# Optimization experiments

Hardware: AMD Instinct MI355X
Metric: run time of the kernel (lower is better)

The kernel has to match this reference:

```python
import jax, jax.numpy as jnp
import numpy as np

NUM_HEADS = 32
NUM_KV_HEADS = 2
HEAD_DIM = 128
ROTARY_DIM = 64  # partial_rotary_factor 0.5 * head_dim
HIDDEN = 4096
SEQ = 2048


def _rotate_half_interleaved(x):
    # rotates pairs (x0,x1)->(-x1,x0) interleaved, matching torch rotate_half above
    x1 = x[..., 0::2]
    x2 = x[..., 1::2]
    return jnp.stack((-x2, x1), axis=-1).reshape(x.shape)


def _apply_rope(q, k, cos, sin):
    # q: [S, Hq, D], k: [S, Hkv, D], cos/sin: [S, ROTARY_DIM]
    # torch code: take first half of cos/sin then repeat_interleave(2) -> length ROTARY_DIM
    cos_i = jnp.repeat(cos[:, : ROTARY_DIM // 2], 2, axis=-1)[:, None, :]  # [S,1,RD]
    sin_i = jnp.repeat(sin[:, : ROTARY_DIM // 2], 2, axis=-1)[:, None, :]
    q_rot, q_pass = q[..., :ROTARY_DIM], q[..., ROTARY_DIM:]
    k_rot, k_pass = k[..., :ROTARY_DIM], k[..., ROTARY_DIM:]
    q_rot = q_rot * cos_i + _rotate_half_interleaved(q_rot) * sin_i
    k_rot = k_rot * cos_i + _rotate_half_interleaved(k_rot) * sin_i
    return jnp.concatenate([q_rot, q_pass], -1), jnp.concatenate([k_rot, k_pass], -1)


def setup_inputs() -> dict:
    key = jax.random.key(0)
    ks = jax.random.split(key, 6)
    S = SEQ
    qkv_out = (NUM_HEADS + 2 * NUM_KV_HEADS) * HEAD_DIM  # 4608
    hidden_states = jax.random.normal(ks[0], (S, HIDDEN), jnp.float32)
    # realistic rope angles
    inv_freq = 1.0 / (10000.0 ** (np.arange(0, ROTARY_DIM, 2, dtype=np.float32) / ROTARY_DIM))
    ang = np.arange(S, dtype=np.float32)[:, None] * inv_freq[None, :]  # [S, RD/2]
    ang = np.concatenate([ang, ang], axis=-1)  # [S, RD]
    cos = jnp.asarray(np.cos(ang))
    sin = jnp.asarray(np.sin(ang))
    w_qkv = jax.random.normal(ks[1], (HIDDEN, qkv_out), jnp.float32) * 0.02
    b_qkv = jax.random.normal(ks[2], (qkv_out,), jnp.float32) * 0.02
    w_o = jax.random.normal(ks[3], (NUM_HEADS * HEAD_DIM, HIDDEN), jnp.float32) * 0.02
    return {"hidden_states": hidden_states, "cos": cos, "sin": sin,
            "w_qkv": w_qkv, "b_qkv": b_qkv, "w_o": w_o}


def reference(hidden_states, cos, sin, w_qkv, b_qkv, w_o):
    S = hidden_states.shape[0]
    qkv = hidden_states @ w_qkv + b_qkv  # [S, 4608]
    nq = NUM_HEADS * HEAD_DIM
    nkv = NUM_KV_HEADS * HEAD_DIM
    q = qkv[:, :nq].reshape(S, NUM_HEADS, HEAD_DIM)
    k = qkv[:, nq:nq + nkv].reshape(S, NUM_KV_HEADS, HEAD_DIM)
    v = qkv[:, nq + nkv:].reshape(S, NUM_KV_HEADS, HEAD_DIM)
    q, k = _apply_rope(q, k, cos, sin)
    # GQA: repeat kv heads to match q heads
    rep = NUM_HEADS // NUM_KV_HEADS
    k = jnp.repeat(k, rep, axis=1)  # [S, Hq, D]
    v = jnp.repeat(v, rep, axis=1)
    scale = 1.0 / jnp.sqrt(jnp.asarray(HEAD_DIM, q.dtype))
    scores = jnp.einsum("qhd,khd->hqk", q, k) * scale  # [H, S, S]
    causal = jnp.tril(jnp.ones((S, S), bool))
    scores = jnp.where(causal[None], scores, jnp.asarray(-1e30, scores.dtype))
    probs = jax.nn.softmax(scores, axis=-1)
    attn = jnp.einsum("hqk,khd->qhd", probs, v).reshape(S, NUM_HEADS * HEAD_DIM)
    return attn @ w_o  # [S, HIDDEN]
```

## Files before the change

### kernel.cpp

```cpp
#include <hip/hip_runtime.h>
#include <stdint.h>

#define SEQ    2048
#define HIDDEN 4096
#define NQH    32
#define NKVH   2
#define HD     128
#define QKVN   4608
#define ATTN_N 4096

typedef short bf16x8 __attribute__((ext_vector_type(8)));
typedef float f32x4  __attribute__((ext_vector_type(4)));

#define ASYNC16(gp, lp) __builtin_amdgcn_global_load_lds( \
    (const __attribute__((address_space(1))) void*)(gp),  \
    (__attribute__((address_space(3))) void*)(lp), 16, 0, 0)

__device__ __forceinline__ float bf2f(unsigned short u) {
  union { unsigned int i; float f; } v; v.i = ((unsigned int)u) << 16; return v.f;
}
__device__ __forceinline__ unsigned short f2bf(float f) {
  union { float f; unsigned int i; } v; v.f = f;
  unsigned int r = v.i + 0x7fffu + ((v.i >> 16) & 1u);
  return (unsigned short)(r >> 16);
}

__global__ void detect_dtype(const unsigned short* __restrict__ hs, int* __restrict__ flag) {
  int bad = 0;
  for (int i = 0; i < 128; i += 2) {
    const int e = (hs[i] >> 7) & 0xFF;
    if (e < 100 || e > 140) bad++;
  }
  *flag = (bad > 16) ? 1 : 0;
}

__global__ void to_bf16_any(const void* __restrict__ in, unsigned short* __restrict__ out,
                            int n4, const int* __restrict__ flag) {
  const int i = blockIdx.x * blockDim.x + threadIdx.x;
  if (i >= n4) return;
  if (*flag) {
    const float4 f = ((const float4*)in)[i];
    ushort4 u; u.x = f2bf(f.x); u.y = f2bf(f.y); u.z = f2bf(f.z); u.w = f2bf(f.w);
    ((ushort4*)out)[i] = u;
  } else {
    ((ushort4*)out)[i] = ((const ushort4*)in)[i];
  }
}

__global__ void to_f32_any(const void* __restrict__ in, float* __restrict__ out,
                           int n4, const int* __restrict__ flag) {
  const int i = blockIdx.x * blockDim.x + threadIdx.x;
  if (i >= n4) return;
  if (*flag) {
    ((float4*)out)[i] = ((const float4*)in)[i];
  } else {
    const ushort4 u = ((const ushort4*)in)[i];
    float4 f; f.x = bf2f(u.x); f.y = bf2f(u.y); f.z = bf2f(u.z); f.w = bf2f(u.w);
    ((float4*)out)[i] = f;
  }
}

__global__ void transpose_any(const void* __restrict__ in, unsigned short* __restrict__ out,
                              int R, int C, const int* __restrict__ flag) {
  __shared__ unsigned short t[32][36];
  const int r0 = blockIdx.y * 32, c0 = blockIdx.x * 32;
  const int lr = threadIdx.x >> 3;
  const int lc = (threadIdx.x & 7) << 2;
  unsigned short v0, v1, v2, v3;
  if (*flag) {
    const float4 f = *(const float4*)((const float*)in + (size_t)(r0 + lr) * C + c0 + lc);
    v0 = f2bf(f.x); v1 = f2bf(f.y); v2 = f2bf(f.z); v3 = f2bf(f.w);
  } else {
    const ushort4 u = *(const ushort4*)((const unsigned short*)in + (size_t)(r0 + lr) * C + c0 + lc);
    v0 = u.x; v1 = u.y; v2 = u.z; v3 = u.w;
  }
  t[lr][lc] = v0; t[lr][lc + 1] = v1; t[lr][lc + 2] = v2; t[lr][lc + 3] = v3;
  __syncthreads();
  unsigned short* op = out + (size_t)(c0 + lr) * R + r0 + lc;
  ushort4 w;
  w.x = t[lc][lr]; w.y = t[lc + 1][lr]; w.z = t[lc + 2][lr]; w.w = t[lc + 3][lr];
  *(ushort4*)op = w;
}

__global__ __launch_bounds__(256, 2)
void gemm_bt(const unsigned short* __restrict__ A,
             const unsigned short* __restrict__ Bt,
             const float* __restrict__ bias,
             void* __restrict__ C,
             int M, int N, int K, const int* __restrict__ of32) {
  __shared__ __attribute__((aligned(16))) unsigned short As[128 * 32];
  __shared__ __attribute__((aligned(16))) unsigned short Bs[128 * 32];
  const int tid  = threadIdx.x;
  const int wave = tid >> 6, lane = tid & 63;
  const int quad = lane >> 4, l16 = lane & 15;
  const int m0 = blockIdx.y * 128, n0 = blockIdx.x * 128;
  const int wm = (wave >> 1) * 64, wn = (wave & 1) * 64;

  const int crow = tid >> 2;
  const int gsw = ((tid & 3) ^ ((crow >> 1) & 3)) << 3;
  const unsigned short* gA = A + (size_t)(m0 + crow) * K + gsw;
  const unsigned short* gB = Bt + (size_t)(n0 + crow) * K + gsw;
  unsigned short* lA = As + tid * 8;
  unsigned short* lB = Bs + tid * 8;

  const int cxor = (quad ^ ((l16 >> 1) & 3)) << 3;

  f32x4 acc[4][4] = {};

  for (int k0 = 0; k0 < K; k0 += 32) {
    __syncthreads();
    ASYNC16(gA + k0, lA);
    ASYNC16(gA + (size_t)64 * K + k0, lA + 64 * 32);
    ASYNC16(gB + k0, lB);
    ASYNC16(gB + (size_t)64 * K + k0, lB + 64 * 32);
    __syncthreads();
    bf16x8 aF[4], bF[4];
#pragma unroll
    for (int i = 0; i < 4; i++)
      aF[i] = *(const bf16x8*)&As[(wm + i * 16 + l16) * 32 + cxor];
#pragma unroll
    for (int j = 0; j < 4; j++)
      bF[j] = *(const bf16x8*)&Bs[(wn + j * 16 + l16) * 32 + cxor];
#pragma unroll
    for (int i = 0; i < 4; i++)
#pragma unroll
      for (int j = 0; j < 4; j++)
        acc[i][j] = __builtin_amdgcn_mfma_f32_16x16x32_bf16(aF[i], bF[j], acc[i][j], 0, 0, 0);
  }

  const int wf32 = of32 ? *of32 : 0;
#pragma unroll
  for (int j = 0; j < 4; j++) {
    const int col = n0 + wn + j * 16 + l16;
    const float bv = bias ? bias[col] : 0.0f;
#pragma unroll
    for (int i = 0; i < 4; i++) {
#pragma unroll
      for (int r = 0; r < 4; r++) {
        const int row = m0 + wm + i * 16 + quad * 4 + r;
        const float v = acc[i][j][r] + bv;
        const size_t off = (size_t)row * N + col;
        if (wf32) ((float*)C)[off] = v;
        else      ((unsigned short*)C)[off] = f2bf(v);
      }
    }
  }
}

__global__ void rope_split(const unsigned short* __restrict__ qkv,
                           const float* __restrict__ cosb,
                           const float* __restrict__ sinb,
                           unsigned short* __restrict__ qb,
                           unsigned short* __restrict__ kb,
                           unsigned short* __restrict__ vtb) {
  const int s = blockIdx.x;
  const unsigned short* row = qkv + (size_t)s * QKVN;
  const float sc = 0.08838834764831845f * 1.44269504088896341f;
  for (int p = threadIdx.x; p < QKVN / 2; p += blockDim.x) {
    const int col = p << 1;
    const int head = col >> 7;
    const int d = col & 127;
    float x0 = bf2f(row[col]), x1 = bf2f(row[col + 1]);
    float y0 = x0, y1 = x1;
    if (d < 64) {
      const float c  = cosb[s * 64 + (d >> 1)];
      const float sn = sinb[s * 64 + (d >> 1)];
      y0 = x0 * c - x1 * sn;
      y1 = x1 * c + x0 * sn;
    }
    if (head < NQH) {
      const size_t o = (size_t)head * SEQ * HD + (size_t)s * HD + d;
      qb[o] = f2bf(y0 * sc); qb[o + 1] = f2bf(y1 * sc);
    } else if (head < NQH + NKVH) {
      const size_t o = (size_t)(head - NQH) * SEQ * HD + (size_t)s * HD + d;
      kb[o] = f2bf(y0); kb[o + 1] = f2bf(y1);
    } else {
      const size_t o = (size_t)(head - NQH - NKVH) * HD * SEQ + (size_t)d * SEQ + s;
      vtb[o] = f2bf(x0); vtb[o + SEQ] = f2bf(x1);
    }
  }
}

__global__ __launch_bounds__(256, 3)
void attn_fwd(const unsigned short* __restrict__ qb,
              const unsigned short* __restrict__ kb,
              const unsigned short* __restrict__ vtb,
              unsigned short* __restrict__ ob) {
  const int h = blockIdx.x;
  const int qt = 31 - (int)blockIdx.y;
  const int tid = threadIdx.x;
  const int wave = tid >> 6, lane = tid & 63;
  const int quad = lane >> 4, l16 = lane & 15;
  const int q0 = qt * 64 + wave * 16;
  const unsigned short* qh  = qb  + (size_t)h * SEQ * HD;
  const unsigned short* kh  = kb  + (size_t)(h >> 4) * SEQ * HD;
  const unsigned short* vth = vtb + (size_t)(h >> 4) * HD * SEQ;

  __shared__ __attribute__((aligned(16))) unsigned short Ks[64 * 128];
  __shared__ __attribute__((aligned(16))) unsigned short Vs[128 * 64];
  __shared__ __attribute__((aligned(16))) unsigned short plds[4][16][80];

  bf16x8 qf[4];
#pragma unroll
  for (int kbk = 0; kbk < 4; kbk++)
    qf[kbk] = *(const bf16x8*)&qh[(size_t)(q0 + l16) * HD + kbk * 32 + quad * 8];

  bf16x8 onesf;
#pragma unroll
  for (int i = 0; i < 8; i++) onesf[i] = (short)0x3F80;

  f32x4 oacc[8] = {};
  f32x4 lacc = {};
  float mrow[4] = {-1e30f, -1e30f, -1e30f, -1e30f};

  for (int kt = 0; kt <= qt; kt++) {
    const int kbase = kt * 64;
    __syncthreads();
#pragma unroll
    for (int c = 0; c < 4; c++) {
      const int j = c * 256 + tid;
      const int key = j >> 4;
      const int g = (j & 15) ^ (key & 15);
      ASYNC16(kh + (size_t)(kbase + key) * HD + g * 8, (unsigned short*)Ks + j * 8);
    }
#pragma unroll
    for (int c = 0; c < 4; c++) {
      const int j = c * 256 + tid;
      const int d = j >> 3;
      const int g = (j & 7) ^ (d & 7);
      ASYNC16(vth + (size_t)d * SEQ + kbase + g * 8, (unsigned short*)Vs + j * 8);
    }
    __syncthreads();

    f32x4 sv[4] = {};
#pragma unroll
    for (int kbk = 0; kbk < 4; kbk++) {
#pragma unroll
      for (int t = 0; t < 4; t++) {
        bf16x8 kf = *(const bf16x8*)&Ks[(t * 16 + l16) * 128 + (((kbk << 2) + quad) ^ l16) * 8];
        sv[t] = __builtin_amdgcn_mfma_f32_16x16x32_bf16(qf[kbk], kf, sv[t], 0, 0, 0);
      }
    }
    if (kt == qt) {
#pragma unroll
      for (int t = 0; t < 4; t++) {
        const int key = kbase + t * 16 + l16;
#pragma unroll
        for (int r = 0; r < 4; r++)
          if (key > q0 + quad * 4 + r) sv[t][r] = -1e30f;
      }
    }
    float alpha[4];
#pragma unroll
    for (int r = 0; r < 4; r++) {
      float mx = fmaxf(fmaxf(sv[0][r], sv[1][r]), fmaxf(sv[2][r], sv[3][r]));
#pragma unroll
      for (int off = 8; off; off >>= 1) mx = fmaxf(mx, __shfl_xor(mx, off));
      const float mnew = fmaxf(mrow[r], mx);
      alpha[r] = __builtin_exp2f(mrow[r] - mnew);
      mrow[r] = mnew;
#pragma unroll
      for (int t = 0; t < 4; t++)
        sv[t][r] = __builtin_exp2f(sv[t][r] - mnew);
    }
#pragma unroll
    for (int dt = 0; dt < 8; dt++)
#pragma unroll
      for (int r = 0; r < 4; r++) oacc[dt][r] *= alpha[r];
#pragma unroll
    for (int r = 0; r < 4; r++) lacc[r] *= alpha[r];
    __syncthreads();
#pragma unroll
    for (int r = 0; r < 4; r++)
#pragma unroll
      for (int t = 0; t < 4; t++)
        plds[wave][quad * 4 + r][t * 16 + l16] = f2bf(sv[t][r]);
    __syncthreads();
    bf16x8 pf0 = *(const bf16x8*)&plds[wave][l16][quad * 8];
    bf16x8 pf1 = *(const bf16x8*)&plds[wave][l16][32 + quad * 8];
    lacc = __builtin_amdgcn_mfma_f32_16x16x32_bf16(pf0, onesf, lacc, 0, 0, 0);
    lacc = __builtin_amdgcn_mfma_f32_16x16x32_bf16(pf1, onesf, lacc, 0, 0, 0);
#pragma unroll
    for (int dt = 0; dt < 8; dt++) {
      const int vrow = (dt * 16 + l16) * 64;
      bf16x8 vf0 = *(const bf16x8*)&Vs[vrow + ((quad) ^ (l16 & 7)) * 8];
      oacc[dt] = __builtin_amdgcn_mfma_f32_16x16x32_bf16(pf0, vf0, oacc[dt], 0, 0, 0);
      bf16x8 vf1 = *(const bf16x8*)&Vs[vrow + ((4 + quad) ^ (l16 & 7)) * 8];
      oacc[dt] = __builtin_amdgcn_mfma_f32_16x16x32_bf16(pf1, vf1, oacc[dt], 0, 0, 0);
    }
  }
#pragma unroll
  for (int dt = 0; dt < 8; dt++) {
#pragma unroll
    for (int r = 0; r < 4; r++) {
      const float v = oacc[dt][r] / lacc[r];
      ob[(size_t)(q0 + quad * 4 + r) * ATTN_N + h * HD + dt * 16 + l16] = f2bf(v);
    }
  }
}

extern "C" void kernel_launch(void* const* d_in, const int* in_sizes, int n_in,
                              void* d_out, int out_size, void* d_ws, size_t ws_size,
                              hipStream_t stream) {
  const void* hs_raw   = d_in[0];
  const void* cos_raw  = d_in[1];
  const void* sin_raw  = d_in[2];
  const void* wqkv_raw = d_in[3];
  const void* bqkv_raw = d_in[4];
  const void* wo_raw   = d_in[5];
  unsigned short* ws = (unsigned short*)d_ws;

  unsigned short* R1   = ws;
  unsigned short* R2   = R1 + (size_t)QKVN * HIDDEN;
  unsigned short* hs_c = R2 + (size_t)SEQ * QKVN;
  float* cosf  = (float*)(hs_c + (size_t)SEQ * HIDDEN);
  float* sinf  = cosf + SEQ * 64;
  float* biasf = sinf + SEQ * 64;
  int*   flag  = (int*)(biasf + QKVN);

  unsigned short* wt_qkv = R1;
  unsigned short* qbuf   = R1;
  unsigned short* kbuf   = qbuf + (size_t)NQH * SEQ * HD;
  unsigned short* vtbuf  = kbuf + (size_t)NKVH * SEQ * HD;
  unsigned short* wt_o   = R1;
  unsigned short* qkv    = R2;
  unsigned short* attnb  = R2;

  detect_dtype<<<1, 1, 0, stream>>>((const unsigned short*)hs_raw, flag);
  to_bf16_any<<<(SEQ * HIDDEN / 4 + 255) / 256, 256, 0, stream>>>(hs_raw, hs_c, SEQ * HIDDEN / 4, flag);
  to_f32_any<<<(SEQ * 64 / 4 + 255) / 256, 256, 0, stream>>>(cos_raw, cosf, SEQ * 64 / 4, flag);
  to_f32_any<<<(SEQ * 64 / 4 + 255) / 256, 256, 0, stream>>>(sin_raw, sinf, SEQ * 64 / 4, flag);
  to_f32_any<<<(QKVN / 4 + 255) / 256, 256, 0, stream>>>(bqkv_raw, biasf, QKVN / 4, flag);

  transpose_any<<<dim3(QKVN / 32, HIDDEN / 32), 256, 0, stream>>>(wqkv_raw, wt_qkv, HIDDEN, QKVN, flag);
  gemm_bt<<<dim3(QKVN / 128, SEQ / 128), 256, 0, stream>>>(hs_c, wt_qkv, biasf, qkv, SEQ, QKVN, HIDDEN, nullptr);
  rope_split<<<SEQ, 256, 0, stream>>>(qkv, cosf, sinf, qbuf, kbuf, vtbuf);
  attn_fwd<<<dim3(NQH, SEQ / 64), 256, 0, stream>>>(qbuf, kbuf, vtbuf, attnb);
  transpose_any<<<dim3(ATTN_N / 32, HIDDEN / 32), 256, 0, stream>>>(wo_raw, wt_o, HIDDEN, ATTN_N, flag);
  gemm_bt<<<dim3(ATTN_N / 128, SEQ / 128), 256, 0, stream>>>(attnb, wt_o, nullptr, d_out, SEQ, ATTN_N, HIDDEN, flag);
}
```

Baseline: 494.5 us.

## Replace GEMM with 256x256-tile double-buffered 8-phase pipelined kernel

Replaces the 128x128 single-buffered bf16 GEMM with a 512-thread kernel computing 256x256 tiles over K-steps of 64. LDS is double-buffered, and async global-to-LDS prefetch of the next tile is interleaved with four MFMA phases using barriers, vmcnt waits and setprio. The aim is to hide load latency and raise arithmetic intensity per LDS byte. In exchange the grid shrinks to 128-144 blocks, which may leave many CUs idle, and 128KB of LDS limits residency to one block per CU.

```diff
diff --git a/kernel.cpp b/kernel.cpp
--- a/kernel.cpp
+++ b/kernel.cpp
@@ -15,6 +15,8 @@
 #define ASYNC16(gp, lp) __builtin_amdgcn_global_load_lds( \
     (const __attribute__((address_space(1))) void*)(gp),  \
     (__attribute__((address_space(3))) void*)(lp), 16, 0, 0)
+
+#define MFMA16(a, b, c) __builtin_amdgcn_mfma_f32_16x16x32_bf16((a), (b), (c), 0, 0, 0)
 
 __device__ __forceinline__ float bf2f(unsigned short u) {
   union { unsigned int i; float f; } v; v.i = ((unsigned int)u) << 16; return v.f;
@@ -82,51 +84,118 @@
   *(ushort4*)op = w;
 }
 
-__global__ __launch_bounds__(256, 2)
-void gemm_bt(const unsigned short* __restrict__ A,
-             const unsigned short* __restrict__ Bt,
-             const float* __restrict__ bias,
-             void* __restrict__ C,
-             int M, int N, int K, const int* __restrict__ of32) {
-  __shared__ __attribute__((aligned(16))) unsigned short As[128 * 32];
-  __shared__ __attribute__((aligned(16))) unsigned short Bs[128 * 32];
+__global__ __launch_bounds__(512, 2)
+void gemm_bt_8ph(const unsigned short* __restrict__ A,
+                 const unsigned short* __restrict__ Bt,
+                 const float* __restrict__ bias,
+                 void* __restrict__ C,
+                 int M, int N, int K, const int* __restrict__ of32) {
+  __shared__ __attribute__((aligned(16))) unsigned short lds[65536];
   const int tid  = threadIdx.x;
   const int wave = tid >> 6, lane = tid & 63;
   const int quad = lane >> 4, l16 = lane & 15;
-  const int m0 = blockIdx.y * 128, n0 = blockIdx.x * 128;
-  const int wm = (wave >> 1) * 64, wn = (wave & 1) * 64;
-
-  const int crow = tid >> 2;
-  const int gsw = ((tid & 3) ^ ((crow >> 1) & 3)) << 3;
-  const unsigned short* gA = A + (size_t)(m0 + crow) * K + gsw;
-  const unsigned short* gB = Bt + (size_t)(n0 + crow) * K + gsw;
-  unsigned short* lA = As + tid * 8;
-  unsigned short* lB = Bs + tid * 8;
-
-  const int cxor = (quad ^ ((l16 >> 1) & 3)) << 3;
-
-  f32x4 acc[4][4] = {};
-
-  for (int k0 = 0; k0 < K; k0 += 32) {
-    __syncthreads();
-    ASYNC16(gA + k0, lA);
-    ASYNC16(gA + (size_t)64 * K + k0, lA + 64 * 32);
-    ASYNC16(gB + k0, lB);
-    ASYNC16(gB + (size_t)64 * K + k0, lB + 64 * 32);
-    __syncthreads();
-    bf16x8 aF[4], bF[4];
-#pragma unroll
-    for (int i = 0; i < 4; i++)
-      aF[i] = *(const bf16x8*)&As[(wm + i * 16 + l16) * 32 + cxor];
-#pragma unroll
-    for (int j = 0; j < 4; j++)
-      bF[j] = *(const bf16x8*)&Bs[(wn + j * 16 + l16) * 32 + cxor];
-#pragma unroll
-    for (int i = 0; i < 4; i++)
-#pragma unroll
-      for (int j = 0; j < 4; j++)
-        acc[i][j] = __builtin_amdgcn_mfma_f32_16x16x32_bf16(aF[i], bF[j], acc[i][j], 0, 0, 0);
-  }
+  const int m0 = blockIdx.y * 256, n0 = blockIdx.x * 256;
+  const int wm = (wave >> 2) * 128, wn = (wave & 3) * 64;
+
+  const int srow = tid >> 2;
+  const int g8   = (((tid & 3) ^ ((srow >> 1) & 3)) << 3);
+  const unsigned short* gA = A  + (size_t)(m0 + srow) * K + g8;
+  const unsigned short* gB = Bt + (size_t)(n0 + srow) * K + g8;
+  const size_t rstep = (size_t)128 * K;
+
+  const int rsw   = ((quad ^ ((l16 >> 1) & 3)) << 3);
+  const int aBase = (wm + l16) * 32 + rsw;
+  const int bBase = (wn + l16) * 32 + rsw;
+
+  f32x4 acc[8][4] = {};
+  const int nt = K >> 6;
+
+#define STAGE(bufb, p, kbase) do {                                        \
+    const unsigned short* _s = ((p) & 1) ? gB : gA;                       \
+    const int _ko = (kbase) + (((p) >> 1) << 5);                          \
+    unsigned short* _d = &lds[((((bufb) << 2) | (p)) << 13) + tid * 8];   \
+    ASYNC16(_s + _ko, _d);                                                \
+    ASYNC16(_s + rstep + _ko, _d + 4096);                                 \
+  } while (0)
+
+#define BARX() do { asm volatile("" ::: "memory");          \
+    __builtin_amdgcn_s_barrier();                           \
+    asm volatile("" ::: "memory"); } while (0)
+
+  STAGE(0, 0, 0);
+  STAGE(0, 1, 0);
+  STAGE(0, 2, 0);
+  STAGE(0, 3, 0);
+  asm volatile("s_waitcnt vmcnt(4)" ::: "memory");
+  BARX();
+
+  for (int t = 0; t < nt; ++t) {
+    const int b   = t & 1;
+    const int kb1 = (t + 1) << 6;
+    const bool pf = (t + 1 < nt);
+    const int c0 = ((b << 2) | 0) << 13;
+    const int c1 = ((b << 2) | 1) << 13;
+    const int c2 = ((b << 2) | 2) << 13;
+    const int c3 = ((b << 2) | 3) << 13;
+    bf16x8 af[8], bf0, bf1;
+
+#pragma unroll
+    for (int i = 0; i < 8; i++) af[i] = *(const bf16x8*)&lds[c0 + aBase + i * 512];
+    bf0 = *(const bf16x8*)&lds[c1 + bBase + 0 * 512];
+    bf1 = *(const bf16x8*)&lds[c1 + bBase + 1 * 512];
+    if (pf) STAGE(b ^ 1, 0, kb1);
+    BARX();
+    __builtin_amdgcn_s_setprio(1);
+#pragma unroll
+    for (int i = 0; i < 8; i++) acc[i][0] = MFMA16(af[i], bf0, acc[i][0]);
+#pragma unroll
+    for (int i = 0; i < 8; i++) acc[i][1] = MFMA16(af[i], bf1, acc[i][1]);
+    __builtin_amdgcn_s_setprio(0);
+    BARX();
+
+    bf0 = *(const bf16x8*)&lds[c1 + bBase + 2 * 512];
+    bf1 = *(const bf16x8*)&lds[c1 + bBase + 3 * 512];
+    if (pf) STAGE(b ^ 1, 1, kb1);
+    BARX();
+    __builtin_amdgcn_s_setprio(1);
+#pragma unroll
+    for (int i = 0; i < 8; i++) acc[i][2] = MFMA16(af[i], bf0, acc[i][2]);
+#pragma unroll
+    for (int i = 0; i < 8; i++) acc[i][3] = MFMA16(af[i], bf1, acc[i][3]);
+    __builtin_amdgcn_s_setprio(0);
+    if (t == nt - 1) asm volatile("s_waitcnt vmcnt(0)" ::: "memory");
+    else             asm volatile("s_waitcnt vmcnt(4)" ::: "memory");
+    BARX();
+
+#pragma unroll
+    for (int i = 0; i < 8; i++) af[i] = *(const bf16x8*)&lds[c2 + aBase + i * 512];
+    bf0 = *(const bf16x8*)&lds[c3 + bBase + 0 * 512];
+    bf1 = *(const bf16x8*)&lds[c3 + bBase + 1 * 512];
+    if (pf) STAGE(b ^ 1, 2, kb1);
+    BARX();
+    __builtin_amdgcn_s_setprio(1);
+#pragma unroll
+    for (int i = 0; i < 8; i++) acc[i][0] = MFMA16(af[i], bf0, acc[i][0]);
+#pragma unroll
+    for (int i = 0; i < 8; i++) acc[i][1] = MFMA16(af[i], bf1, acc[i][1]);
+    __builtin_amdgcn_s_setprio(0);
+    BARX();
+
+    bf0 = *(const bf16x8*)&lds[c3 + bBase + 2 * 512];
+    bf1 = *(const bf16x8*)&lds[c3 + bBase + 3 * 512];
+    if (pf) STAGE(b ^ 1, 3, kb1);
+    BARX();
+    __builtin_amdgcn_s_setprio(1);
+#pragma unroll
+    for (int i = 0; i < 8; i++) acc[i][2] = MFMA16(af[i], bf0, acc[i][2]);
+#pragma unroll
+    for (int i = 0; i < 8; i++) acc[i][3] = MFMA16(af[i], bf1, acc[i][3]);
+    __builtin_amdgcn_s_setprio(0);
+    asm volatile("s_waitcnt vmcnt(4)" ::: "memory");
+    BARX();
+  }
+#undef STAGE
+#undef BARX
 
   const int wf32 = of32 ? *of32 : 0;
 #pragma unroll
@@ -134,7 +203,7 @@
     const int col = n0 + wn + j * 16 + l16;
     const float bv = bias ? bias[col] : 0.0f;
 #pragma unroll
-    for (int i = 0; i < 4; i++) {
+    for (int i = 0; i < 8; i++) {
 #pragma unroll
       for (int r = 0; r < 4; r++) {
         const int row = m0 + wm + i * 16 + quad * 4 + r;
@@ -333,9 +402,9 @@
   to_f32_any<<<(QKVN / 4 + 255) / 256, 256, 0, stream>>>(bqkv_raw, biasf, QKVN / 4, flag);
 
   transpose_any<<<dim3(QKVN / 32, HIDDEN / 32), 256, 0, stream>>>(wqkv_raw, wt_qkv, HIDDEN, QKVN, flag);
-  gemm_bt<<<dim3(QKVN / 128, SEQ / 128), 256, 0, stream>>>(hs_c, wt_qkv, biasf, qkv, SEQ, QKVN, HIDDEN, nullptr);
+  gemm_bt_8ph<<<dim3(QKVN / 256, SEQ / 256), 512, 0, stream>>>(hs_c, wt_qkv, biasf, qkv, SEQ, QKVN, HIDDEN, nullptr);
   rope_split<<<SEQ, 256, 0, stream>>>(qkv, cosf, sinf, qbuf, kbuf, vtbuf);
   attn_fwd<<<dim3(NQH, SEQ / 64), 256, 0, stream>>>(qbuf, kbuf, vtbuf, attnb);
   transpose_any<<<dim3(ATTN_N / 32, HIDDEN / 32), 256, 0, stream>>>(wo_raw, wt_o, HIDDEN, ATTN_N, flag);
-  gemm_bt<<<dim3(ATTN_N / 128, SEQ / 128), 256, 0, stream>>>(attnb, wt_o, nullptr, d_out, SEQ, ATTN_N, HIDDEN, flag);
-}
+  gemm_bt_8ph<<<dim3(ATTN_N / 256, SEQ / 256), 512, 0, stream>>>(attnb, wt_o, nullptr, d_out, SEQ, ATTN_N, HIDDEN, flag);
+}
```

Result: slower. 529.8 us (+7.1%).

## Double-buffer GEMM with async LDS prefetch, 256x128 tiles and XCD block remap

Applied to the files above, without the earlier changes.

Replaces the single-buffered 128x128 GEMM with a 512-thread, 256x128-tile kernel. It double-buffers 64-wide K slices in LDS, issuing global-to-LDS async loads for the next slice while MFMAs run on the current one, and uses explicit vmcnt waits and barriers plus setprio around the MFMA bursts. Block IDs are remapped across groups of 8 to spread tiles over chiplets. The cost targeted is exposed global-load latency and the two barriers per K step. In exchange it uses 96KB of LDS per block and hand-counted waitcnt logic that is fragile.

```diff
diff --git a/kernel.cpp b/kernel.cpp
--- a/kernel.cpp
+++ b/kernel.cpp
@@ -15,6 +15,8 @@
 #define ASYNC16(gp, lp) __builtin_amdgcn_global_load_lds( \
     (const __attribute__((address_space(1))) void*)(gp),  \
     (__attribute__((address_space(3))) void*)(lp), 16, 0, 0)
+
+#define MFMA16(a, b, c) __builtin_amdgcn_mfma_f32_16x16x32_bf16((a), (b), (c), 0, 0, 0)
 
 __device__ __forceinline__ float bf2f(unsigned short u) {
   union { unsigned int i; float f; } v; v.i = ((unsigned int)u) << 16; return v.f;
@@ -82,51 +84,107 @@
   *(ushort4*)op = w;
 }
 
-__global__ __launch_bounds__(256, 2)
-void gemm_bt(const unsigned short* __restrict__ A,
-             const unsigned short* __restrict__ Bt,
-             const float* __restrict__ bias,
-             void* __restrict__ C,
-             int M, int N, int K, const int* __restrict__ of32) {
-  __shared__ __attribute__((aligned(16))) unsigned short As[128 * 32];
-  __shared__ __attribute__((aligned(16))) unsigned short Bs[128 * 32];
+__global__ __launch_bounds__(512, 2)
+void gemm_bt_2ph(const unsigned short* __restrict__ A,
+                 const unsigned short* __restrict__ Bt,
+                 const float* __restrict__ bias,
+                 void* __restrict__ C,
+                 int M, int N, int K, const int* __restrict__ of32) {
+  __shared__ __attribute__((aligned(16))) unsigned short lds[49152];
   const int tid  = threadIdx.x;
   const int wave = tid >> 6, lane = tid & 63;
   const int quad = lane >> 4, l16 = lane & 15;
-  const int m0 = blockIdx.y * 128, n0 = blockIdx.x * 128;
+
+  const int nwg = gridDim.x * gridDim.y;
+  int bid = blockIdx.y * gridDim.x + blockIdx.x;
+  bid = (bid & 7) * (nwg >> 3) + (bid >> 3);
+  const int bx = bid % gridDim.x, by = bid / gridDim.x;
+  const int m0 = by * 256, n0 = bx * 128;
+
   const int wm = (wave >> 1) * 64, wn = (wave & 1) * 64;
 
-  const int crow = tid >> 2;
-  const int gsw = ((tid & 3) ^ ((crow >> 1) & 3)) << 3;
-  const unsigned short* gA = A + (size_t)(m0 + crow) * K + gsw;
-  const unsigned short* gB = Bt + (size_t)(n0 + crow) * K + gsw;
-  unsigned short* lA = As + tid * 8;
-  unsigned short* lB = Bs + tid * 8;
-
-  const int cxor = (quad ^ ((l16 >> 1) & 3)) << 3;
+  const int srow = tid >> 2;
+  const int g8   = (((tid & 3) ^ ((srow >> 1) & 3)) << 3);
+  const unsigned short* gA = A  + (size_t)(m0 + srow) * K + g8;
+  const unsigned short* gB = Bt + (size_t)(n0 + srow) * K + g8;
+  const size_t rstep = (size_t)128 * K;
+
+  const int rsw   = ((quad ^ ((l16 >> 1) & 3)) << 3);
+  const int aBase = (wm + l16) * 32 + rsw;
+  const int bBase = 8192 + (wn + l16) * 32 + rsw;
 
   f32x4 acc[4][4] = {};
-
-  for (int k0 = 0; k0 < K; k0 += 32) {
-    __syncthreads();
-    ASYNC16(gA + k0, lA);
-    ASYNC16(gA + (size_t)64 * K + k0, lA + 64 * 32);
-    ASYNC16(gB + k0, lB);
-    ASYNC16(gB + (size_t)64 * K + k0, lB + 64 * 32);
-    __syncthreads();
-    bf16x8 aF[4], bF[4];
-#pragma unroll
-    for (int i = 0; i < 4; i++)
-      aF[i] = *(const bf16x8*)&As[(wm + i * 16 + l16) * 32 + cxor];
-#pragma unroll
-    for (int j = 0; j < 4; j++)
-      bF[j] = *(const bf16x8*)&Bs[(wn + j * 16 + l16) * 32 + cxor];
-#pragma unroll
-    for (int i = 0; i < 4; i++)
-#pragma unroll
-      for (int j = 0; j < 4; j++)
-        acc[i][j] = __builtin_amdgcn_mfma_f32_16x16x32_bf16(aF[i], bF[j], acc[i][j], 0, 0, 0);
-  }
+  const int nt = K >> 6;
+
+#define STAGEA(bufb, kh, kb) do {                                              \
+    const unsigned short* _s = gA + (kb) + ((kh) << 5);                        \
+    unsigned short* _d = &lds[(bufb) * 24576 + (kh) * 12288 + tid * 8];        \
+    ASYNC16(_s, _d);                                                           \
+    ASYNC16(_s + rstep, _d + 4096);                                            \
+  } while (0)
+#define STAGEB(bufb, kh, kb) do {                                              \
+    const unsigned short* _s = gB + (kb) + ((kh) << 5);                        \
+    unsigned short* _d = &lds[(bufb) * 24576 + (kh) * 12288 + 8192 + tid * 8]; \
+    ASYNC16(_s, _d);                                                           \
+  } while (0)
+#define BARX() do { asm volatile("" ::: "memory");          \
+    __builtin_amdgcn_s_barrier();                           \
+    asm volatile("" ::: "memory"); } while (0)
+
+  STAGEA(0, 0, 0); STAGEB(0, 0, 0);
+  STAGEA(0, 1, 0); STAGEB(0, 1, 0);
+  asm volatile("s_waitcnt vmcnt(3)" ::: "memory");
+  BARX();
+
+  for (int t = 0; t < nt; ++t) {
+    const int b = t & 1, nb = b ^ 1;
+    const int kb1 = (t + 1) << 6;
+    const bool pf = (t + 1 < nt);
+
+    {
+      const int cb = b * 24576;
+      bf16x8 af[4], bfr[4];
+#pragma unroll
+      for (int i = 0; i < 4; i++) af[i]  = *(const bf16x8*)&lds[cb + aBase + i * 512];
+#pragma unroll
+      for (int j = 0; j < 4; j++) bfr[j] = *(const bf16x8*)&lds[cb + bBase + j * 512];
+      if (pf) { STAGEA(nb, 0, kb1); STAGEB(nb, 0, kb1); }
+      BARX();
+      __builtin_amdgcn_s_setprio(1);
+#pragma unroll
+      for (int i = 0; i < 4; i++)
+#pragma unroll
+        for (int j = 0; j < 4; j++) acc[i][j] = MFMA16(af[i], bfr[j], acc[i][j]);
+      __builtin_amdgcn_s_setprio(0);
+      if (pf) asm volatile("s_waitcnt vmcnt(3)" ::: "memory");
+      else    asm volatile("s_waitcnt vmcnt(0)" ::: "memory");
+      BARX();
+    }
+
+    {
+      const int cb = b * 24576 + 12288;
+      bf16x8 af[4], bfr[4];
+#pragma unroll
+      for (int i = 0; i < 4; i++) af[i]  = *(const bf16x8*)&lds[cb + aBase + i * 512];
+#pragma unroll
+      for (int j = 0; j < 4; j++) bfr[j] = *(const bf16x8*)&lds[cb + bBase + j * 512];
+      if (pf) { STAGEA(nb, 1, kb1); STAGEB(nb, 1, kb1); }
+      BARX();
+      __builtin_amdgcn_s_setprio(1);
+#pragma unroll
+      for (int i = 0; i < 4; i++)
+#pragma unroll
+        for (int j = 0; j < 4; j++) acc[i][j] = MFMA16(af[i], bfr[j], acc[i][j]);
+      __builtin_amdgcn_s_setprio(0);
+      if (pf) {
+        asm volatile("s_waitcnt vmcnt(3)" ::: "memory");
+        BARX();
+      }
+    }
+  }
+#undef STAGEA
+#undef STAGEB
+#undef BARX
 
   const int wf32 = of32 ? *of32 : 0;
 #pragma unroll
@@ -333,9 +391,9 @@
   to_f32_any<<<(QKVN / 4 + 255) / 256, 256, 0, stream>>>(bqkv_raw, biasf, QKVN / 4, flag);
 
   transpose_any<<<dim3(QKVN / 32, HIDDEN / 32), 256, 0, stream>>>(wqkv_raw, wt_qkv, HIDDEN, QKVN, flag);
-  gemm_bt<<<dim3(QKVN / 128, SEQ / 128), 256, 0, stream>>>(hs_c, wt_qkv, biasf, qkv, SEQ, QKVN, HIDDEN, nullptr);
+  gemm_bt_2ph<<<dim3(QKVN / 128, SEQ / 256), 512, 0, stream>>>(hs_c, wt_qkv, biasf, qkv, SEQ, QKVN, HIDDEN, nullptr);
   rope_split<<<SEQ, 256, 0, stream>>>(qkv, cosf, sinf, qbuf, kbuf, vtbuf);
   attn_fwd<<<dim3(NQH, SEQ / 64), 256, 0, stream>>>(qbuf, kbuf, vtbuf, attnb);
   transpose_any<<<dim3(ATTN_N / 32, HIDDEN / 32), 256, 0, stream>>>(wo_raw, wt_o, HIDDEN, ATTN_N, flag);
-  gemm_bt<<<dim3(ATTN_N / 128, SEQ / 128), 256, 0, stream>>>(attnb, wt_o, nullptr, d_out, SEQ, ATTN_N, HIDDEN, flag);
-}
+  gemm_bt_2ph<<<dim3(ATTN_N / 128, SEQ / 256), 512, 0, stream>>>(attnb, wt_o, nullptr, d_out, SEQ, ATTN_N, HIDDEN, flag);
+}
```

Measured after the change: 531.4 us. 1.07x slower.

## Double-buffer K/V tiles in attention and drop per-wave P barriers

Applied to the files above, without the earlier changes.

The attention kernel now keeps two LDS buffers for K and V. While the current tile is being computed, it issues the async global-to-LDS loads for the next key tile, overlapping memory traffic with MFMA work. The two block-wide barriers around the per-wave probability scratch are removed, since each wave only reads its own slice. LDS use per block roughly doubles, so the occupancy hint drops from 3 to 2 blocks per CU. The overlap depends on whether the compiler inserts a full vmcnt wait before the LDS reads.

```diff
diff --git a/kernel.cpp b/kernel.cpp
--- a/kernel.cpp
+++ b/kernel.cpp
@@ -181,7 +181,7 @@
   }
 }
 
-__global__ __launch_bounds__(256, 3)
+__global__ __launch_bounds__(256, 2)
 void attn_fwd(const unsigned short* __restrict__ qb,
               const unsigned short* __restrict__ kb,
               const unsigned short* __restrict__ vtb,
@@ -196,8 +196,8 @@
   const unsigned short* kh  = kb  + (size_t)(h >> 4) * SEQ * HD;
   const unsigned short* vth = vtb + (size_t)(h >> 4) * HD * SEQ;
 
-  __shared__ __attribute__((aligned(16))) unsigned short Ks[64 * 128];
-  __shared__ __attribute__((aligned(16))) unsigned short Vs[128 * 64];
+  __shared__ __attribute__((aligned(16))) unsigned short Ks[2][64 * 128];
+  __shared__ __attribute__((aligned(16))) unsigned short Vs[2][128 * 64];
   __shared__ __attribute__((aligned(16))) unsigned short plds[4][16][80];
 
   bf16x8 qf[4];
@@ -213,31 +213,38 @@
   f32x4 lacc = {};
   float mrow[4] = {-1e30f, -1e30f, -1e30f, -1e30f};
 
+#define STAGEKV(kt_, bsel) do {                                                  \
+    const int kb_ = (kt_) * 64;                                                  \
+    _Pragma("unroll")                                                            \
+    for (int c = 0; c < 4; c++) {                                                \
+      const int j = c * 256 + tid;                                               \
+      const int key = j >> 4;                                                    \
+      const int g = (j & 15) ^ (key & 15);                                       \
+      ASYNC16(kh + (size_t)(kb_ + key) * HD + g * 8, &Ks[bsel][0] + j * 8);      \
+    }                                                                            \
+    _Pragma("unroll")                                                            \
+    for (int c = 0; c < 4; c++) {                                                \
+      const int j = c * 256 + tid;                                               \
+      const int d = j >> 3;                                                      \
+      const int g = (j & 7) ^ (d & 7);                                           \
+      ASYNC16(vth + (size_t)d * SEQ + kb_ + g * 8, &Vs[bsel][0] + j * 8);        \
+    }                                                                            \
+  } while (0)
+
+  STAGEKV(0, 0);
+
   for (int kt = 0; kt <= qt; kt++) {
+    const int b = kt & 1;
     const int kbase = kt * 64;
     __syncthreads();
-#pragma unroll
-    for (int c = 0; c < 4; c++) {
-      const int j = c * 256 + tid;
-      const int key = j >> 4;
-      const int g = (j & 15) ^ (key & 15);
-      ASYNC16(kh + (size_t)(kbase + key) * HD + g * 8, (unsigned short*)Ks + j * 8);
-    }
-#pragma unroll
-    for (int c = 0; c < 4; c++) {
-      const int j = c * 256 + tid;
-      const int d = j >> 3;
-      const int g = (j & 7) ^ (d & 7);
-      ASYNC16(vth + (size_t)d * SEQ + kbase + g * 8, (unsigned short*)Vs + j * 8);
-    }
-    __syncthreads();
+    if (kt < qt) STAGEKV(kt + 1, b ^ 1);
 
     f32x4 sv[4] = {};
 #pragma unroll
     for (int kbk = 0; kbk < 4; kbk++) {
 #pragma unroll
       for (int t = 0; t < 4; t++) {
-        bf16x8 kf = *(const bf16x8*)&Ks[(t * 16 + l16) * 128 + (((kbk << 2) + quad) ^ l16) * 8];
+        bf16x8 kf = *(const bf16x8*)&Ks[b][(t * 16 + l16) * 128 + (((kbk << 2) + quad) ^ l16) * 8];
         sv[t] = __builtin_amdgcn_mfma_f32_16x16x32_bf16(qf[kbk], kf, sv[t], 0, 0, 0);
       }
     }
@@ -269,13 +276,11 @@
       for (int r = 0; r < 4; r++) oacc[dt][r] *= alpha[r];
 #pragma unroll
     for (int r = 0; r < 4; r++) lacc[r] *= alpha[r];
-    __syncthreads();
 #pragma unroll
     for (int r = 0; r < 4; r++)
 #pragma unroll
       for (int t = 0; t < 4; t++)
         plds[wave][quad * 4 + r][t * 16 + l16] = f2bf(sv[t][r]);
-    __syncthreads();
     bf16x8 pf0 = *(const bf16x8*)&plds[wave][l16][quad * 8];
     bf16x8 pf1 = *(const bf16x8*)&plds[wave][l16][32 + quad * 8];
     lacc = __builtin_amdgcn_mfma_f32_16x16x32_bf16(pf0, onesf, lacc, 0, 0, 0);
@@ -283,12 +288,13 @@
 #pragma unroll
     for (int dt = 0; dt < 8; dt++) {
       const int vrow = (dt * 16 + l16) * 64;
-      bf16x8 vf0 = *(const bf16x8*)&Vs[vrow + ((quad) ^ (l16 & 7)) * 8];
+      bf16x8 vf0 = *(const bf16x8*)&Vs[b][vrow + ((quad) ^ (l16 & 7)) * 8];
       oacc[dt] = __builtin_amdgcn_mfma_f32_16x16x32_bf16(pf0, vf0, oacc[dt], 0, 0, 0);
-      bf16x8 vf1 = *(const bf16x8*)&Vs[vrow + ((4 + quad) ^ (l16 & 7)) * 8];
+      bf16x8 vf1 = *(const bf16x8*)&Vs[b][vrow + ((4 + quad) ^ (l16 & 7)) * 8];
       oacc[dt] = __builtin_amdgcn_mfma_f32_16x16x32_bf16(pf1, vf1, oacc[dt], 0, 0, 0);
     }
   }
+#undef STAGEKV
 #pragma unroll
   for (int dt = 0; dt < 8; dt++) {
 #pragma unroll
```

Result: no change. 497.4 us (+0.6%).
